# Kernel tuning notes

Measured on AMD Instinct MI355X. Metric: run time of the kernel, lower is better.

## Reference

```python
import jax, jax.numpy as jnp
import numpy as np

FORGET_BIAS = 1.0  # BasicLSTMCell default


def setup_inputs() -> dict:
    key = jax.random.key(0)
    k1, k2 = jax.random.split(key)
    B, T, F, H = 64, 128, 1024, 1024
    x = jax.random.normal(k1, (B, T, F), dtype=jnp.float32)
    # BasicLSTMCell kernel: [F + H, 4H], init uniform(-0.1, 0.1); bias zeros
    W = jax.random.uniform(k2, (F + H, 4 * H), dtype=jnp.float32, minval=-0.1, maxval=0.1)
    b = jnp.zeros((4 * H,), dtype=jnp.float32)
    return {"x": x, "W": W, "b": b}


def reference(x, W, b):
    # x: [B, T, F]; W: [F+H, 4H]; b: [4H]
    B, T, F = x.shape
    H = W.shape[1] // 4

    def step(carry, xt):
        c, h = carry  # [B, H] each
        z = jnp.concatenate([xt, h], axis=-1) @ W + b  # [B, 4H]
        i, j, f, o = jnp.split(z, 4, axis=-1)
        new_c = c * jax.nn.sigmoid(f + FORGET_BIAS) + jax.nn.sigmoid(i) * jnp.tanh(j)
        new_h = jnp.tanh(new_c) * jax.nn.sigmoid(o)
        return (new_c, new_h), new_h

    c0 = jnp.zeros((B, H), dtype=x.dtype)
    h0 = jnp.zeros((B, H), dtype=x.dtype)
    xs = jnp.swapaxes(x, 0, 1)  # [T, B, F]
    _, ys = jax.lax.scan(step, (c0, h0), xs)  # ys: [T, B, H]
    return jnp.swapaxes(ys, 0, 1)  # [B, T, H] (return_last=False, return_seq_2d=False)
```

## Files before the change

kernel.cpp:

```cpp
#include <hip/hip_runtime.h>
#include <stdint.h>

#define BATCH 64
#define TSEQ  128
#define FDIM  1024
#define HDIM  1024
#define GDIM  4096
#define MROWS 8192
#define NB    128

typedef short bf16x8 __attribute__((ext_vector_type(8)));
typedef float f32x4  __attribute__((ext_vector_type(4)));

__device__ __forceinline__ unsigned short f2bf(float f) {
    union { float f; uint32_t u; } v; v.f = f;
    uint32_t u = v.u;
    return (unsigned short)((u + 0x7FFFu + ((u >> 16) & 1u)) >> 16);
}
__device__ __forceinline__ float bf2f(unsigned short h) {
    union { uint32_t u; float f; } v; v.u = ((uint32_t)h) << 16; return v.f;
}
__device__ __forceinline__ float sigmoidf_(float x) { return 1.f / (1.f + __expf(-x)); }
__device__ __forceinline__ float tanhf_(float x)    { return 2.f / (1.f + __expf(-2.f * x)) - 1.f; }

union SP { short s[8]; int4 v; };
union UU { int4 i; bf16x8 v; };

__device__ __forceinline__ void st64cc(void* p, unsigned long long v) {
    __hip_atomic_store((unsigned long long*)p, v, __ATOMIC_RELAXED, __HIP_MEMORY_SCOPE_AGENT);
}
__device__ __forceinline__ void st32cc(void* p, uint32_t v) {
    __hip_atomic_store((uint32_t*)p, v, __ATOMIC_RELAXED, __HIP_MEMORY_SCOPE_AGENT);
}

__global__ void k_init(uint32_t* p, int nwords) {
    int i = blockIdx.x * blockDim.x + threadIdx.x;
    int s = gridDim.x * blockDim.x;
    for (; i < nwords; i += s) p[i] = 0;
}

__global__ void k_tw(const float* __restrict__ W,
                     unsigned short* __restrict__ wxth, unsigned short* __restrict__ wxtl,
                     unsigned short* __restrict__ wht) {
    __shared__ float tile[64 * 65];
    const int nb = blockIdx.x;
    const int kb = blockIdx.y;
    const int t  = threadIdx.x;
    const int col = t & 63, rg = t >> 6;
#pragma unroll
    for (int i = 0; i < 16; i++) {
        int row = rg * 16 + i;
        tile[row * 65 + col] = W[(size_t)(kb * 64 + row) * 4096 + nb * 64 + col];
    }
    __syncthreads();
    if (kb < 16) {
        const int kbase = kb * 64;
#pragma unroll
        for (int i = 0; i < 16; i++) {
            int rp = rg * 16 + i;
            float v = tile[col * 65 + rp];
            unsigned short h = f2bf(v);
            size_t idx = (size_t)(nb * 64 + rp) * 1024 + kbase + col;
            wxth[idx] = h;
            wxtl[idx] = f2bf(v - bf2f(h));
        }
    } else {
        const int kbase = (kb - 16) * 64;
#pragma unroll
        for (int i = 0; i < 16; i++) {
            int rp = rg * 16 + i;
            float v = tile[col * 65 + rp];
            wht[(size_t)(nb * 64 + rp) * 1024 + kbase + col] = f2bf(v);
        }
    }
}

__global__ __launch_bounds__(256) void k_gemm1(const float* __restrict__ Xf,
                                               const unsigned short* __restrict__ WxTh,
                                               const unsigned short* __restrict__ WxTl,
                                               float* __restrict__ xz) {
    __shared__ short Ash[128 * 40];
    __shared__ short Asl[128 * 40];
    __shared__ short Bsh[128 * 40];
    __shared__ short Bsl[128 * 40];
    const int n0 = blockIdx.x * 128;
    const int m0 = blockIdx.y * 128;
    const int t = threadIdx.x;
    const int wave = t >> 6, lane = t & 63;
    const int wm = wave >> 1, wn = wave & 1;
    const int q = lane >> 4, cl = lane & 15;
    const int row_a = t >> 2;
    const int kc = (t & 3) * 8;

    f32x4 acc[4][4];
#pragma unroll
    for (int i = 0; i < 4; i++)
#pragma unroll
        for (int j = 0; j < 4; j++) acc[i][j] = (f32x4){0.f, 0.f, 0.f, 0.f};

    for (int kb = 0; kb < 32; kb++) {
        const int k0 = kb * 32;
        float va0[8], va1[8];
        {
            const float* p0 = Xf + (size_t)(m0 + row_a) * 1024 + k0 + kc;
            const float* p1 = Xf + (size_t)(m0 + 64 + row_a) * 1024 + k0 + kc;
            *(float4*)(va0)     = *(const float4*)(p0);
            *(float4*)(va0 + 4) = *(const float4*)(p0 + 4);
            *(float4*)(va1)     = *(const float4*)(p1);
            *(float4*)(va1 + 4) = *(const float4*)(p1 + 4);
        }
        int4 bh0 = *(const int4*)(WxTh + (size_t)(n0 + row_a)      * 1024 + k0 + kc);
        int4 bh1 = *(const int4*)(WxTh + (size_t)(n0 + 64 + row_a) * 1024 + k0 + kc);
        int4 bl0 = *(const int4*)(WxTl + (size_t)(n0 + row_a)      * 1024 + k0 + kc);
        int4 bl1 = *(const int4*)(WxTl + (size_t)(n0 + 64 + row_a) * 1024 + k0 + kc);
        __syncthreads();
        {
            SP h0, l0, h1, l1;
#pragma unroll
            for (int i = 0; i < 8; i++) {
                unsigned short h = f2bf(va0[i]);
                h0.s[i] = (short)h; l0.s[i] = (short)f2bf(va0[i] - bf2f(h));
                unsigned short g = f2bf(va1[i]);
                h1.s[i] = (short)g; l1.s[i] = (short)f2bf(va1[i] - bf2f(g));
            }
            *(int4*)(Ash + row_a * 40 + kc)        = h0.v;
            *(int4*)(Asl + row_a * 40 + kc)        = l0.v;
            *(int4*)(Ash + (64 + row_a) * 40 + kc) = h1.v;
            *(int4*)(Asl + (64 + row_a) * 40 + kc) = l1.v;
        }
        *(int4*)(Bsh + row_a * 40 + kc)        = bh0;
        *(int4*)(Bsh + (64 + row_a) * 40 + kc) = bh1;
        *(int4*)(Bsl + row_a * 40 + kc)        = bl0;
        *(int4*)(Bsl + (64 + row_a) * 40 + kc) = bl1;
        __syncthreads();
        bf16x8 ah[4], al[4], bh[4], bl[4];
#pragma unroll
        for (int i = 0; i < 4; i++) {
            ah[i] = *(const bf16x8*)(Ash + (wm * 64 + i * 16 + cl) * 40 + q * 8);
            al[i] = *(const bf16x8*)(Asl + (wm * 64 + i * 16 + cl) * 40 + q * 8);
        }
#pragma unroll
        for (int j = 0; j < 4; j++) {
            bh[j] = *(const bf16x8*)(Bsh + (wn * 64 + j * 16 + cl) * 40 + q * 8);
            bl[j] = *(const bf16x8*)(Bsl + (wn * 64 + j * 16 + cl) * 40 + q * 8);
        }
#pragma unroll
        for (int i = 0; i < 4; i++)
#pragma unroll
            for (int j = 0; j < 4; j++) {
                acc[i][j] = __builtin_amdgcn_mfma_f32_16x16x32_bf16(ah[i], bh[j], acc[i][j], 0, 0, 0);
                acc[i][j] = __builtin_amdgcn_mfma_f32_16x16x32_bf16(al[i], bh[j], acc[i][j], 0, 0, 0);
                acc[i][j] = __builtin_amdgcn_mfma_f32_16x16x32_bf16(ah[i], bl[j], acc[i][j], 0, 0, 0);
            }
    }
#pragma unroll
    for (int i = 0; i < 4; i++) {
#pragma unroll
        for (int j = 0; j < 4; j++) {
            int gm = m0 + wm * 64 + i * 16 + q * 4;
            int gn = n0 + wn * 64 + j * 16 + cl;
#pragma unroll
            for (int r = 0; r < 4; r++)
                xz[(size_t)(gm + r) * 4096 + gn] = acc[i][j][r];
        }
    }
}

__global__ __launch_bounds__(256, 1) void k_rnn(const float* __restrict__ xz,
                                                const unsigned short* __restrict__ WhT,
                                                const float* __restrict__ bias,
                                                unsigned short* hrot,
                                                int* flags,
                                                float* __restrict__ out) {
    __shared__ short Ws[32 * 1024];
    __shared__ short hs[64 * 8];
    const int t = threadIdx.x;
    const int blk = blockIdx.x;
    const int n0 = (((blk & 7) << 4) | (blk >> 3)) * 8;
    const int wave = t >> 6, lane = t & 63;
    const int q = lane >> 4, cl = lane & 15;
    const int m = wave * 16 + cl;

    {
        const int vcol = t >> 3;
        const int part = t & 7;
        const int g = vcol >> 3, cc2 = vcol & 7, swl = vcol & 7;
        const unsigned short* src = WhT + (size_t)(g * 1024 + n0 + cc2) * 1024;
        short* dstrow = Ws + vcol * 1024;
#pragma unroll
        for (int i = 0; i < 16; i++) {
            int kch = part * 16 + i;
            int4 v = *(const int4*)(src + kch * 8);
            *(int4*)(dstrow + ((kch ^ swl) * 8)) = v;
        }
    }
    const int cc = cl & 7;
    const bool act = (cl < 8);
    float bi = 0.f, bj = 0.f, bfv = 0.f, bo = 0.f;
    if (act) {
        bi  = bias[n0 + cc];
        bj  = bias[1024 + n0 + cc];
        bfv = bias[2048 + n0 + cc];
        bo  = bias[3072 + n0 + cc];
    }
    float c[4] = {0.f, 0.f, 0.f, 0.f};
    const int sw = cl & 7;
    const unsigned long long selfmask =
        (t == (blk >> 1)) ? ((blk & 1) ? (1ULL << 32) : 1ULL) : 0ULL;
    __syncthreads();

    for (int tt = 0; tt < TSEQ; tt++) {
        float pxi[4], pxj[4], pxf[4], pxo[4];
        if (act) {
#pragma unroll
            for (int r = 0; r < 4; r++) {
                int m2 = wave * 16 + q * 4 + r;
                const float* xp = xz + (size_t)(m2 * 128 + tt) * 4096 + n0 + cc;
                pxi[r] = xp[0];
                pxj[r] = xp[1024];
                pxf[r] = xp[2048];
                pxo[r] = xp[3072];
            }
        }
        __builtin_amdgcn_sched_barrier(0);
        if (tt > 0) {
            if (t < 64) {
                const unsigned long long* fp =
                    (const unsigned long long*)flags + (size_t)(tt - 1) * 64 + t;
                unsigned long long v;
                do {
                    v = __hip_atomic_load(fp, __ATOMIC_RELAXED, __HIP_MEMORY_SCOPE_AGENT);
                } while (!__all((v | selfmask) == 0x0000000100000001ULL));
            }
            __syncthreads();
        }
        const char* ab = (const char*)hrot + (size_t)tt * 131072 + (size_t)m * 2048 + q * 16;
        UU aa[32];
#pragma unroll
        for (int kb = 0; kb < 32; kb++) aa[kb].i = *(const int4*)(ab + kb * 64);
        __builtin_amdgcn_sched_barrier(0);

        f32x4 acc0a = (f32x4){0.f, 0.f, 0.f, 0.f};
        f32x4 acc0b = (f32x4){0.f, 0.f, 0.f, 0.f};
        f32x4 acc1a = (f32x4){0.f, 0.f, 0.f, 0.f};
        f32x4 acc1b = (f32x4){0.f, 0.f, 0.f, 0.f};
#pragma unroll
        for (int kb = 0; kb < 32; kb += 2) {
            const int ch0 = (kb * 4 + q) ^ sw;
            const int ch1 = ((kb + 1) * 4 + q) ^ sw;
            bf16x8 b00 = *(const bf16x8*)(Ws + cl * 1024 + ch0 * 8);
            bf16x8 b10 = *(const bf16x8*)(Ws + (16 + cl) * 1024 + ch0 * 8);
            bf16x8 b01 = *(const bf16x8*)(Ws + cl * 1024 + ch1 * 8);
            bf16x8 b11 = *(const bf16x8*)(Ws + (16 + cl) * 1024 + ch1 * 8);
            acc0a = __builtin_amdgcn_mfma_f32_16x16x32_bf16(aa[kb].v,     b00, acc0a, 0, 0, 0);
            acc1a = __builtin_amdgcn_mfma_f32_16x16x32_bf16(aa[kb].v,     b10, acc1a, 0, 0, 0);
            acc0b = __builtin_amdgcn_mfma_f32_16x16x32_bf16(aa[kb + 1].v, b01, acc0b, 0, 0, 0);
            acc1b = __builtin_amdgcn_mfma_f32_16x16x32_bf16(aa[kb + 1].v, b11, acc1b, 0, 0, 0);
        }
        f32x4 acc0 = acc0a + acc0b;
        f32x4 acc1 = acc1a + acc1b;
        float zi[4], zj[4], zf[4], zo[4];
#pragma unroll
        for (int r = 0; r < 4; r++) {
            float a0 = acc0[r], a1 = acc1[r];
            float a0x = __shfl_xor(a0, 8);
            float a1x = __shfl_xor(a1, 8);
            zi[r] = a0; zj[r] = a0x; zf[r] = a1; zo[r] = a1x;
        }
        float hv4[4];
        if (act) {
#pragma unroll
            for (int r = 0; r < 4; r++) {
                float vi = zi[r] + pxi[r] + bi;
                float vj = zj[r] + pxj[r] + bj;
                float vf = zf[r] + pxf[r] + bfv + 1.0f;
                float vo = zo[r] + pxo[r] + bo;
                float cn = c[r] * sigmoidf_(vf) + sigmoidf_(vi) * tanhf_(vj);
                c[r] = cn;
                float h = tanhf_(cn) * sigmoidf_(vo);
                hv4[r] = h;
                hs[(wave * 16 + q * 4 + r) * 8 + cc] = (short)f2bf(h);
            }
        }
        __syncthreads();
        if (t < 128) {
            unsigned long long hv = *(const unsigned long long*)(hs + (t >> 1) * 8 + (t & 1) * 4);
            st64cc((char*)hrot + (size_t)(tt + 1) * 131072 + (size_t)(t >> 1) * 2048 + n0 * 2 + (t & 1) * 8, hv);
        }
        __syncthreads();
        if (t == 0) st32cc(flags + (size_t)tt * NB + blk, 1u);
        if (act) {
#pragma unroll
            for (int r = 0; r < 4; r++) {
                int m2 = wave * 16 + q * 4 + r;
                out[(size_t)(m2 * 128 + tt) * 1024 + n0 + cc] = hv4[r];
            }
        }
    }
}

extern "C" void kernel_launch(void* const* d_in, const int* in_sizes, int n_in,
                              void* d_out, int out_size, void* d_ws, size_t ws_size,
                              hipStream_t stream) {
    const float* x = (const float*)d_in[0];
    const float* W = (const float*)d_in[1];
    const float* b = (const float*)d_in[2];
    float* out = (float*)d_out;
    char* ws = (char*)d_ws;

    unsigned short* WXTH = (unsigned short*)(ws);
    unsigned short* WXTL = (unsigned short*)(ws + (size_t)8  * 1024 * 1024);
    unsigned short* WHT  = (unsigned short*)(ws + (size_t)16 * 1024 * 1024);
    float*          XZ   = (float*)         (ws + (size_t)24 * 1024 * 1024);
    int*            FLAGS= (int*)           (ws + (size_t)152 * 1024 * 1024);
    unsigned short* HROT = (unsigned short*)(ws + (size_t)152 * 1024 * 1024 + 65536);

    k_init<<<256, 256, 0, stream>>>((uint32_t*)FLAGS, 49152);
    dim3 gtw(64, 32);
    k_tw<<<gtw, 256, 0, stream>>>(W, WXTH, WXTL, WHT);
    dim3 gg(32, 64);
    k_gemm1<<<gg, 256, 0, stream>>>(x, WXTH, WXTL, XZ);
    k_rnn<<<NB, 256, 0, stream>>>(XZ, WHT, b, HROT, FLAGS, out);
}
```

Baseline: 1.063 ms.

## Consume hidden-state chunks as producer groups finish instead of waiting for all

Replaces the block-wide wait for all 128 producer flags with a per-wave loop that polls the flags and works out which of 8 k-chunk groups are complete. Each complete group's slice of h is loaded and its MFMAs run right away, so the recurrent GEMM overlaps with producers that are still writing. Flag slots are permuted (idx_self) so that each group of 16 producer blocks maps to one contiguous 8-lane byte in the ballot. The costs are extra polling traffic, the removal of the __syncthreads after the wait, and reliance on only a signal fence for acquire ordering, which may be a memory-ordering risk.

After: 1.099 ms. 1.03x slower.

```diff
diff --git a/kernel.cpp b/kernel.cpp
--- a/kernel.cpp
+++ b/kernel.cpp
@@ -205,8 +205,9 @@
     }
     float c[4] = {0.f, 0.f, 0.f, 0.f};
     const int sw = cl & 7;
+    const int idx_self = ((blk & 7) << 4) | (blk >> 3);
     const unsigned long long selfmask =
-        (t == (blk >> 1)) ? ((blk & 1) ? (1ULL << 32) : 1ULL) : 0ULL;
+        ((t & 63) == (idx_self >> 1)) ? ((idx_self & 1) ? (1ULL << 32) : 1ULL) : 0ULL;
     __syncthreads();
 
     for (int tt = 0; tt < TSEQ; tt++) {
@@ -223,39 +224,63 @@
             }
         }
         __builtin_amdgcn_sched_barrier(0);
-        if (tt > 0) {
-            if (t < 64) {
-                const unsigned long long* fp =
-                    (const unsigned long long*)flags + (size_t)(tt - 1) * 64 + t;
-                unsigned long long v;
-                do {
-                    v = __hip_atomic_load(fp, __ATOMIC_RELAXED, __HIP_MEMORY_SCOPE_AGENT);
-                } while (!__all((v | selfmask) == 0x0000000100000001ULL));
-            }
-            __syncthreads();
-        }
+
         const char* ab = (const char*)hrot + (size_t)tt * 131072 + (size_t)m * 2048 + q * 16;
-        UU aa[32];
-#pragma unroll
-        for (int kb = 0; kb < 32; kb++) aa[kb].i = *(const int4*)(ab + kb * 64);
-        __builtin_amdgcn_sched_barrier(0);
+        const unsigned long long* fbase =
+            (const unsigned long long*)flags + (size_t)(tt - 1) * 64 + (t & 63);
 
         f32x4 acc0a = (f32x4){0.f, 0.f, 0.f, 0.f};
         f32x4 acc0b = (f32x4){0.f, 0.f, 0.f, 0.f};
         f32x4 acc1a = (f32x4){0.f, 0.f, 0.f, 0.f};
         f32x4 acc1b = (f32x4){0.f, 0.f, 0.f, 0.f};
-#pragma unroll
-        for (int kb = 0; kb < 32; kb += 2) {
-            const int ch0 = (kb * 4 + q) ^ sw;
-            const int ch1 = ((kb + 1) * 4 + q) ^ sw;
-            bf16x8 b00 = *(const bf16x8*)(Ws + cl * 1024 + ch0 * 8);
-            bf16x8 b10 = *(const bf16x8*)(Ws + (16 + cl) * 1024 + ch0 * 8);
-            bf16x8 b01 = *(const bf16x8*)(Ws + cl * 1024 + ch1 * 8);
-            bf16x8 b11 = *(const bf16x8*)(Ws + (16 + cl) * 1024 + ch1 * 8);
-            acc0a = __builtin_amdgcn_mfma_f32_16x16x32_bf16(aa[kb].v,     b00, acc0a, 0, 0, 0);
-            acc1a = __builtin_amdgcn_mfma_f32_16x16x32_bf16(aa[kb].v,     b10, acc1a, 0, 0, 0);
-            acc0b = __builtin_amdgcn_mfma_f32_16x16x32_bf16(aa[kb + 1].v, b01, acc0b, 0, 0, 0);
-            acc1b = __builtin_amdgcn_mfma_f32_16x16x32_bf16(aa[kb + 1].v, b11, acc1b, 0, 0, 0);
+
+        unsigned done = 0;
+        while (done != 0xFFu) {
+            unsigned ready;
+            if (tt == 0) {
+                ready = 0xFFu;
+            } else {
+                unsigned long long v =
+                    __hip_atomic_load(fbase, __ATOMIC_RELAXED, __HIP_MEMORY_SCOPE_AGENT);
+                unsigned long long x = __ballot((v | selfmask) == 0x0000000100000001ULL);
+                x &= x >> 1; x &= x >> 2; x &= x >> 4;
+                ready = 0;
+#pragma unroll
+                for (int g2 = 0; g2 < 8; g2++)
+                    ready |= (unsigned)((x >> (8 * g2)) & 1ULL) << g2;
+            }
+            unsigned avail = ready & ~done;
+            while (avail) {
+                const int g = __builtin_ctz(avail);
+                avail &= avail - 1;
+                done |= 1u << g;
+                __atomic_signal_fence(__ATOMIC_ACQUIRE);
+                UU a0, a1, a2, a3;
+                a0.i = *(const int4*)(ab + (4 * g + 0) * 64);
+                a1.i = *(const int4*)(ab + (4 * g + 1) * 64);
+                a2.i = *(const int4*)(ab + (4 * g + 2) * 64);
+                a3.i = *(const int4*)(ab + (4 * g + 3) * 64);
+                const int ch0 = ((4 * g + 0) * 4 + q) ^ sw;
+                const int ch1 = ((4 * g + 1) * 4 + q) ^ sw;
+                const int ch2 = ((4 * g + 2) * 4 + q) ^ sw;
+                const int ch3 = ((4 * g + 3) * 4 + q) ^ sw;
+                bf16x8 b00 = *(const bf16x8*)(Ws + cl * 1024 + ch0 * 8);
+                bf16x8 b10 = *(const bf16x8*)(Ws + (16 + cl) * 1024 + ch0 * 8);
+                bf16x8 b01 = *(const bf16x8*)(Ws + cl * 1024 + ch1 * 8);
+                bf16x8 b11 = *(const bf16x8*)(Ws + (16 + cl) * 1024 + ch1 * 8);
+                acc0a = __builtin_amdgcn_mfma_f32_16x16x32_bf16(a0.v, b00, acc0a, 0, 0, 0);
+                acc1a = __builtin_amdgcn_mfma_f32_16x16x32_bf16(a0.v, b10, acc1a, 0, 0, 0);
+                acc0b = __builtin_amdgcn_mfma_f32_16x16x32_bf16(a1.v, b01, acc0b, 0, 0, 0);
+                acc1b = __builtin_amdgcn_mfma_f32_16x16x32_bf16(a1.v, b11, acc1b, 0, 0, 0);
+                bf16x8 b02 = *(const bf16x8*)(Ws + cl * 1024 + ch2 * 8);
+                bf16x8 b12 = *(const bf16x8*)(Ws + (16 + cl) * 1024 + ch2 * 8);
+                bf16x8 b03 = *(const bf16x8*)(Ws + cl * 1024 + ch3 * 8);
+                bf16x8 b13 = *(const bf16x8*)(Ws + (16 + cl) * 1024 + ch3 * 8);
+                acc0a = __builtin_amdgcn_mfma_f32_16x16x32_bf16(a2.v, b02, acc0a, 0, 0, 0);
+                acc1a = __builtin_amdgcn_mfma_f32_16x16x32_bf16(a2.v, b12, acc1a, 0, 0, 0);
+                acc0b = __builtin_amdgcn_mfma_f32_16x16x32_bf16(a3.v, b03, acc0b, 0, 0, 0);
+                acc1b = __builtin_amdgcn_mfma_f32_16x16x32_bf16(a3.v, b13, acc1b, 0, 0, 0);
+            }
         }
         f32x4 acc0 = acc0a + acc0b;
         f32x4 acc1 = acc1a + acc1b;
@@ -288,7 +313,7 @@
             st64cc((char*)hrot + (size_t)(tt + 1) * 131072 + (size_t)(t >> 1) * 2048 + n0 * 2 + (t & 1) * 8, hv);
         }
         __syncthreads();
-        if (t == 0) st32cc(flags + (size_t)tt * NB + blk, 1u);
+        if (t == 0) st32cc(flags + (size_t)tt * NB + idx_self, 1u);
         if (act) {
 #pragma unroll
             for (int r = 0; r < 4; r++) {
```

## Keep recurrent weight slice in registers instead of LDS across timesteps

Applied to the files above, without the earlier changes.

Each wave now loads its slice of the recurrent weight matrix straight from global memory into 64 bf16x8 register vectors once, before the time loop. The shared-memory staging, the swizzled LDS reads inside the per-step MFMA loop and the initial __syncthreads are removed. This takes the LDS read latency off the serial recurrence critical path. The cost is 256 extra VGPRs per thread, which risks spilling, and the selfmask test now matches a thread in every wave instead of only wave 0.

Result: no change. 1.058 ms (-0.4%).

```diff
diff --git a/kernel.cpp b/kernel.cpp
--- a/kernel.cpp
+++ b/kernel.cpp
@@ -172,7 +172,6 @@
                                                 unsigned short* hrot,
                                                 int* flags,
                                                 float* __restrict__ out) {
-    __shared__ short Ws[32 * 1024];
     __shared__ short hs[64 * 8];
     const int t = threadIdx.x;
     const int blk = blockIdx.x;
@@ -181,19 +180,6 @@
     const int q = lane >> 4, cl = lane & 15;
     const int m = wave * 16 + cl;
 
-    {
-        const int vcol = t >> 3;
-        const int part = t & 7;
-        const int g = vcol >> 3, cc2 = vcol & 7, swl = vcol & 7;
-        const unsigned short* src = WhT + (size_t)(g * 1024 + n0 + cc2) * 1024;
-        short* dstrow = Ws + vcol * 1024;
-#pragma unroll
-        for (int i = 0; i < 16; i++) {
-            int kch = part * 16 + i;
-            int4 v = *(const int4*)(src + kch * 8);
-            *(int4*)(dstrow + ((kch ^ swl) * 8)) = v;
-        }
-    }
     const int cc = cl & 7;
     const bool act = (cl < 8);
     float bi = 0.f, bj = 0.f, bfv = 0.f, bo = 0.f;
@@ -203,11 +189,26 @@
         bfv = bias[2048 + n0 + cc];
         bo  = bias[3072 + n0 + cc];
     }
+
+    bf16x8 B0[32], B1[32];
+    {
+        const unsigned short* bsrc0 =
+            WhT + (size_t)((cl >> 3) * 1024 + n0 + (cl & 7)) * 1024 + q * 8;
+        const unsigned short* bsrc1 =
+            WhT + (size_t)((2 + (cl >> 3)) * 1024 + n0 + (cl & 7)) * 1024 + q * 8;
+#pragma unroll
+        for (int kb = 0; kb < 32; kb++) {
+            UU u0, u1;
+            u0.i = *(const int4*)(bsrc0 + kb * 32);
+            u1.i = *(const int4*)(bsrc1 + kb * 32);
+            B0[kb] = u0.v;
+            B1[kb] = u1.v;
+        }
+    }
+
     float c[4] = {0.f, 0.f, 0.f, 0.f};
-    const int sw = cl & 7;
     const unsigned long long selfmask =
-        (t == (blk >> 1)) ? ((blk & 1) ? (1ULL << 32) : 1ULL) : 0ULL;
-    __syncthreads();
+        ((t & 63) == (blk >> 1)) ? ((blk & 1) ? (1ULL << 32) : 1ULL) : 0ULL;
 
     for (int tt = 0; tt < TSEQ; tt++) {
         float pxi[4], pxj[4], pxf[4], pxo[4];
@@ -246,16 +247,10 @@
         f32x4 acc1b = (f32x4){0.f, 0.f, 0.f, 0.f};
 #pragma unroll
         for (int kb = 0; kb < 32; kb += 2) {
-            const int ch0 = (kb * 4 + q) ^ sw;
-            const int ch1 = ((kb + 1) * 4 + q) ^ sw;
-            bf16x8 b00 = *(const bf16x8*)(Ws + cl * 1024 + ch0 * 8);
-            bf16x8 b10 = *(const bf16x8*)(Ws + (16 + cl) * 1024 + ch0 * 8);
-            bf16x8 b01 = *(const bf16x8*)(Ws + cl * 1024 + ch1 * 8);
-            bf16x8 b11 = *(const bf16x8*)(Ws + (16 + cl) * 1024 + ch1 * 8);
-            acc0a = __builtin_amdgcn_mfma_f32_16x16x32_bf16(aa[kb].v,     b00, acc0a, 0, 0, 0);
-            acc1a = __builtin_amdgcn_mfma_f32_16x16x32_bf16(aa[kb].v,     b10, acc1a, 0, 0, 0);
-            acc0b = __builtin_amdgcn_mfma_f32_16x16x32_bf16(aa[kb + 1].v, b01, acc0b, 0, 0, 0);
-            acc1b = __builtin_amdgcn_mfma_f32_16x16x32_bf16(aa[kb + 1].v, b11, acc1b, 0, 0, 0);
+            acc0a = __builtin_amdgcn_mfma_f32_16x16x32_bf16(aa[kb].v,     B0[kb],     acc0a, 0, 0, 0);
+            acc1a = __builtin_amdgcn_mfma_f32_16x16x32_bf16(aa[kb].v,     B1[kb],     acc1a, 0, 0, 0);
+            acc0b = __builtin_amdgcn_mfma_f32_16x16x32_bf16(aa[kb + 1].v, B0[kb + 1], acc0b, 0, 0, 0);
+            acc1b = __builtin_amdgcn_mfma_f32_16x16x32_bf16(aa[kb + 1].v, B1[kb + 1], acc1b, 0, 0, 0);
         }
         f32x4 acc0 = acc0a + acc0b;
         f32x4 acc1 = acc1a + acc1b;
```
